# Optimization experiments

Hardware: AMD Instinct MI355X
Metric: run time of the kernel (lower is better)

The kernel has to match this reference:

```python
import jax, jax.numpy as jnp
import numpy as np

B, C, L = 4, 512, 4096

def setup_inputs() -> dict:
    key = jax.random.key(0)
    k1, k2, k3, k4 = jax.random.split(key, 4)
    proj_query = jax.random.normal(k1, (B, C, L), dtype=jnp.float32)
    proj_key = jax.random.normal(k2, (B, C, L), dtype=jnp.float32)
    proj_val = jax.random.normal(k3, (B, C, L), dtype=jnp.float32)
    # binary padding mask over key positions, broadcast over query axis
    padding_mask = (jax.random.uniform(k4, (B, 1, L)) < 0.9).astype(jnp.float32)
    return {"proj_query": proj_query, "proj_key": proj_key,
            "proj_val": proj_val, "padding_mask": padding_mask}

def reference(proj_query, proj_key, proj_val, padding_mask):
    c = proj_query.shape[1]
    # energy[b,i,j] = sum_c Q[b,c,i] * K[b,c,j]  -> (B, L1, L2)
    energy = jnp.einsum('bci,bcj->bij', proj_query, proj_key)
    attention = energy / jnp.sqrt(jnp.asarray(c, dtype=energy.dtype))
    attention = attention + jnp.log(padding_mask + 1e-6)
    attention = jax.nn.softmax(attention, axis=-1)
    attention = attention * padding_mask
    attention = attention.transpose(0, 2, 1)  # (B, L2, L1)
    out = jnp.einsum('bcj,bji->bci', proj_val, attention)  # (B, C, L1)
    return out, attention
```

## Files before the change

kernel.cpp:

```cpp
#include <hip/hip_runtime.h>

#define B_ 4
#define C_ 512
#define L_ 4096

typedef __attribute__((ext_vector_type(8))) short bf16x8;
typedef __attribute__((ext_vector_type(4))) float f32x4;

#define MFMA16(a, b, c) __builtin_amdgcn_mfma_f32_16x16x32_bf16(a, b, c, 0, 0, 0)

static __device__ __forceinline__ unsigned short f2bf_rne(float f) {
  unsigned u = __float_as_uint(f);
  u += 0x7FFFu + ((u >> 16) & 1u);
  return (unsigned short)(u >> 16);
}
static __device__ __forceinline__ unsigned pack_rne(float a, float b) {
  return (unsigned)f2bf_rne(a) | ((unsigned)f2bf_rne(b) << 16);
}
static __device__ __forceinline__ float bflo2f(unsigned w) {
  return __uint_as_float(w << 16);
}
static __device__ __forceinline__ float bfhi2f(unsigned w) {
  return __uint_as_float(w & 0xFFFF0000u);
}

static __device__ __forceinline__ void g2lds16(const unsigned short* g,
                                               unsigned short* l) {
  __builtin_amdgcn_global_load_lds(
      (const __attribute__((address_space(1))) unsigned int*)g,
      (__attribute__((address_space(3))) unsigned int*)l, 16, 0, 0);
}

__global__ __launch_bounds__(256) void transpose_cast_k(
    const float* __restrict__ Q, const float* __restrict__ K,
    unsigned short* __restrict__ Qt, unsigned short* __restrict__ Kt) {
  int zb = blockIdx.z;
  int b = zb >> 1;
  const float* src = ((zb & 1) ? K : Q) + (size_t)b * C_ * L_;
  unsigned short* dst = ((zb & 1) ? Kt : Qt) + (size_t)b * L_ * C_;
  int i0 = blockIdx.x * 64, c0 = blockIdx.y * 64;
  __shared__ float tile[64][65];
  int t = threadIdx.x;
  int cr = t >> 2, ig = (t & 3) * 16;
  const float* s = src + (size_t)(c0 + cr) * L_ + i0 + ig;
#pragma unroll
  for (int q = 0; q < 4; ++q) {
    float4 v = *(const float4*)(s + 4 * q);
    tile[cr][ig + 4 * q + 0] = v.x;
    tile[cr][ig + 4 * q + 1] = v.y;
    tile[cr][ig + 4 * q + 2] = v.z;
    tile[cr][ig + 4 * q + 3] = v.w;
  }
  __syncthreads();
  int ir = t >> 2, cg = (t & 3) * 16;
  unsigned wds[8];
#pragma unroll
  for (int k = 0; k < 8; ++k)
    wds[k] = pack_rne(tile[cg + 2 * k][ir], tile[cg + 2 * k + 1][ir]);
  unsigned short* d = dst + (size_t)(i0 + ir) * C_ + c0 + cg;
  uint4 o0, o1;
  o0.x = wds[0]; o0.y = wds[1]; o0.z = wds[2]; o0.w = wds[3];
  o1.x = wds[4]; o1.y = wds[5]; o1.z = wds[6]; o1.w = wds[7];
  *(uint4*)d = o0;
  *(uint4*)(d + 8) = o1;
}

__global__ __launch_bounds__(256) void cast_v_k(
    const float* __restrict__ V, const float* __restrict__ mask,
    unsigned short* __restrict__ Vb) {
  size_t idx = ((size_t)blockIdx.x * 256 + threadIdx.x) * 8;
  int b = (int)(idx >> 21);
  int j = (int)(idx & (L_ - 1));
  float4 v0 = *(const float4*)(V + idx);
  float4 v1 = *(const float4*)(V + idx + 4);
  const float* m = mask + (size_t)b * L_ + j;
  float4 m0 = *(const float4*)m;
  float4 m1 = *(const float4*)(m + 4);
  uint4 o;
  o.x = pack_rne(v0.x * m0.x, v0.y * m0.y);
  o.y = pack_rne(v0.z * m0.z, v0.w * m0.w);
  o.z = pack_rne(v1.x * m1.x, v1.y * m1.y);
  o.w = pack_rne(v1.z * m1.z, v1.w * m1.w);
  *(uint4*)(Vb + idx) = o;
}

__device__ __forceinline__ void gemm_8phase(
    const unsigned short* __restrict__ Ab,
    const unsigned short* __restrict__ Bb, int lda, int ldb, int Kdim,
    unsigned short* sA, unsigned short* sB, f32x4 (&acc)[8][4]) {
  const int t = threadIdx.x;
  const int lane = t & 63;
  const int quad = lane >> 4;
  const int l15 = lane & 15;
  const int w = t >> 6;
  const int wm = (w & 1) * 128;
  const int wn = (w >> 1) * 64;
  const int et = (t * 8) ^ (((t >> 5) & 1) << 4);
  const int srw = et >> 5;
  const int scl = et & 31;
  const int nt = Kdim >> 6;

  auto stage = [&](int nom, int hh) {
    int st = nom < nt ? nom : nt - 1;
    int db = nom & 1;
    int h = hh & 1;
    const unsigned short* g;
    unsigned short* l;
    if (hh < 2) {
      g = Bb + (size_t)(h * 128 + srw) * ldb + st * 64 + scl;
      l = sB + db * 16384 + h * 4096 + t * 8;
    } else {
      g = Ab + (size_t)(h * 128 + srw) * lda + st * 64 + scl;
      l = sA + db * 16384 + h * 4096 + t * 8;
    }
    g2lds16(g, l);
    g2lds16(g + 32, l + 8192);
  };
  auto rd = [&](const unsigned short* s, int db, int kc, int row) -> bf16x8 {
    int e = db * 16384 + kc * 8192 + row * 32 + quad * 8;
    e ^= ((e >> 8) & 1) << 4;
    return *(const bf16x8*)(s + e);
  };

  bf16x8 aF[4][2], b0[2][2], b1[2][2];
  auto rdA4 = [&](int db, int mbase) {
#pragma unroll
    for (int m = 0; m < 4; ++m)
#pragma unroll
      for (int kc = 0; kc < 2; ++kc)
        aF[m][kc] = rd(sA, db, kc, wm + (mbase + m) * 16 + l15);
  };
  auto rdB2 = [&](bf16x8 (&bf)[2][2], int db, int nbase) {
#pragma unroll
    for (int n = 0; n < 2; ++n)
#pragma unroll
      for (int kc = 0; kc < 2; ++kc)
        bf[n][kc] = rd(sB, db, kc, wn + (nbase + n) * 16 + l15);
  };
  auto mfma8 = [&](bf16x8 (&bf)[2][2], int mo, int no) {
    __builtin_amdgcn_s_setprio(1);
#pragma unroll
    for (int m = 0; m < 4; ++m)
#pragma unroll
      for (int n = 0; n < 2; ++n) {
        acc[mo + m][no + n] = MFMA16(aF[m][0], bf[n][0], acc[mo + m][no + n]);
        acc[mo + m][no + n] = MFMA16(aF[m][1], bf[n][1], acc[mo + m][no + n]);
      }
    __builtin_amdgcn_s_setprio(0);
  };

#define BAR_() __builtin_amdgcn_s_barrier()
#define LGKM0_() asm volatile("s_waitcnt lgkmcnt(0)" ::: "memory")
#define VM6_() asm volatile("s_waitcnt vmcnt(6)" ::: "memory")
#define SCHED0_() __builtin_amdgcn_sched_barrier(0)

  stage(0, 0); stage(0, 1); stage(0, 2); stage(0, 3);
  asm volatile("s_waitcnt vmcnt(4)" ::: "memory");
  stage(1, 0); stage(1, 1); stage(1, 2);
  asm volatile("s_waitcnt vmcnt(6)" ::: "memory");
  BAR_();

  const int ni = nt >> 1;
  for (int i = 0; i < ni; ++i) {
    const int X = 2 * i;
    rdA4(0, 0); rdB2(b0, 0, 0); rdB2(b1, 0, 2);
    stage(X + 1, 3);
    BAR_(); LGKM0_();
    mfma8(b0, 0, 0);
    BAR_();
    stage(X + 2, 0);
    BAR_();
    mfma8(b1, 0, 2);
    BAR_();
    rdA4(0, 4);
    stage(X + 2, 1);
    BAR_(); LGKM0_();
    mfma8(b0, 4, 0);
    BAR_();
    stage(X + 2, 2);
    VM6_(); BAR_();
    mfma8(b1, 4, 2);
    BAR_(); SCHED0_();
    rdA4(1, 0); rdB2(b0, 1, 0); rdB2(b1, 1, 2);
    stage(X + 2, 3);
    BAR_(); LGKM0_();
    mfma8(b0, 0, 0);
    BAR_();
    stage(X + 3, 0);
    BAR_();
    mfma8(b1, 0, 2);
    BAR_();
    rdA4(1, 4);
    stage(X + 3, 1);
    BAR_(); LGKM0_();
    mfma8(b0, 4, 0);
    BAR_();
    stage(X + 3, 2);
    VM6_(); BAR_();
    mfma8(b1, 4, 2);
    BAR_(); SCHED0_();
  }
  asm volatile("s_waitcnt vmcnt(0)" ::: "memory");
}

__global__ __launch_bounds__(512, 2) void gemm1_8p_k(
    const unsigned short* __restrict__ Qt, const unsigned short* __restrict__ Kt,
    const float* __restrict__ mask, unsigned short* __restrict__ t0,
    unsigned short* __restrict__ t1, unsigned short* __restrict__ t2,
    unsigned short* __restrict__ t3, float* __restrict__ rowsum) {
  __shared__ unsigned short sA[32768];
  __shared__ unsigned short sB[32768];
  int flat = blockIdx.x + (blockIdx.y << 4) + (blockIdx.z << 8);
  int swz = (flat & 7) * 128 + (flat >> 3);
  int bx = swz & 15, by = (swz >> 4) & 15, b = swz >> 8;
  unsigned short* tbb = (b == 0) ? t0 : (b == 1) ? t1 : (b == 2) ? t2 : t3;
  int i0 = by * 256, j0 = bx * 256;
  f32x4 acc[8][4] = {};
  gemm_8phase(Qt + (size_t)b * L_ * C_ + (size_t)i0 * C_,
              Kt + (size_t)b * L_ * C_ + (size_t)j0 * C_, C_, C_, C_, sA, sB,
              acc);
  int t = threadIdx.x;
  int lane = t & 63;
  int quad = lane >> 4;
  int l15 = lane & 15;
  int w = t >> 6;
  int wm = (w & 1) * 128;
  int wn = (w >> 1) * 64;
  const float scale = 0.04419417382415922f;
  float lm[4], mv[4];
#pragma unroll
  for (int n = 0; n < 4; ++n) {
    int j = j0 + wn + n * 16 + l15;
    float m = mask[(size_t)b * L_ + j];
    mv[n] = m;
    lm[n] = __logf(m + 1e-6f);
  }
  float rs[8][4];
#pragma unroll
  for (int m = 0; m < 8; ++m)
#pragma unroll
    for (int r = 0; r < 4; ++r) rs[m][r] = 0.f;
#pragma unroll
  for (int m = 0; m < 8; ++m) {
    int irow = i0 + wm + m * 16 + quad * 4;
#pragma unroll
    for (int r = 0; r < 4; ++r) {
      size_t ro = (size_t)(irow + r) * L_;
#pragma unroll
      for (int n = 0; n < 4; ++n) {
        float x = fminf(acc[m][n][r] * scale + lm[n], 60.f);
        float tv = __expf(x);
        rs[m][r] += tv;
        tbb[ro + j0 + wn + n * 16 + l15] = f2bf_rne(tv * mv[n]);
      }
    }
  }
#pragma unroll
  for (int mm = 1; mm < 16; mm <<= 1)
#pragma unroll
    for (int m = 0; m < 8; ++m)
#pragma unroll
      for (int r = 0; r < 4; ++r) rs[m][r] += __shfl_xor(rs[m][r], mm, 64);
  if (l15 == 0) {
    float* rb = rowsum + (size_t)b * L_ + i0 + wm;
#pragma unroll
    for (int m = 0; m < 8; ++m)
#pragma unroll
      for (int r = 0; r < 4; ++r)
        atomicAdd(&rb[m * 16 + quad * 4 + r], rs[m][r]);
  }
}

__global__ __launch_bounds__(512, 2) void gemm2_8p_k(
    const unsigned short* __restrict__ Vb, const unsigned short* __restrict__ t0,
    const unsigned short* __restrict__ t1, const unsigned short* __restrict__ t2,
    const unsigned short* __restrict__ t3, const float* __restrict__ rowsum,
    float* __restrict__ out, float* __restrict__ out2) {
  __shared__ unsigned short sA[32768];
  __shared__ unsigned short sB[32768];
  int flat = blockIdx.x + (blockIdx.y << 4) + (blockIdx.z << 5);
  int swz = (flat & 7) * 32 + (flat >> 3);
  int ix = swz & 15, cy = (swz >> 4) & 1, z = swz >> 5;
  int b = z & 3, ks = z >> 2;
  const unsigned short* tbb =
      (b == 0) ? t0 : (b == 1) ? t1 : (b == 2) ? t2 : t3;
  int i0 = ix * 256, c0 = cy * 256;
  f32x4 acc[8][4] = {};
  gemm_8phase(Vb + (size_t)b * C_ * L_ + (size_t)c0 * L_ + ks * (L_ / 2),
              tbb + (size_t)i0 * L_ + ks * (L_ / 2), L_, L_, L_ / 2, sA, sB,
              acc);
  int t = threadIdx.x;
  int lane = t & 63;
  int quad = lane >> 4;
  int l15 = lane & 15;
  int w = t >> 6;
  int wm = (w & 1) * 128;
  int wn = (w >> 1) * 64;
  float invv[4];
#pragma unroll
  for (int n = 0; n < 4; ++n)
    invv[n] = 1.0f / rowsum[(size_t)b * L_ + i0 + wn + n * 16 + l15];
  float* ob = (ks ? out2 : out) + (size_t)b * C_ * L_;
#pragma unroll
  for (int m = 0; m < 8; ++m) {
    int crow = c0 + wm + m * 16 + quad * 4;
#pragma unroll
    for (int r = 0; r < 4; ++r) {
      size_t ro = (size_t)(crow + r) * L_;
#pragma unroll
      for (int n = 0; n < 4; ++n)
        ob[ro + i0 + wn + n * 16 + l15] = acc[m][n][r] * invv[n];
    }
  }
}

__global__ __launch_bounds__(256) void combine_out_k(
    float* __restrict__ out, const float* __restrict__ out2) {
  size_t idx = ((size_t)blockIdx.x * 256 + threadIdx.x) * 8;
  float4 a0 = *(const float4*)(out + idx);
  float4 a1 = *(const float4*)(out + idx + 4);
  float4 b0 = *(const float4*)(out2 + idx);
  float4 b1 = *(const float4*)(out2 + idx + 4);
  a0.x += b0.x; a0.y += b0.y; a0.z += b0.z; a0.w += b0.w;
  a1.x += b1.x; a1.y += b1.y; a1.z += b1.z; a1.w += b1.w;
  *(float4*)(out + idx) = a0;
  *(float4*)(out + idx + 4) = a1;
}

__global__ __launch_bounds__(256) void finalize_all_k(
    const unsigned short* __restrict__ tb, const float* __restrict__ rowsum,
    float* __restrict__ attn) {
  int b = blockIdx.z;
  const unsigned short* src = tb + (size_t)b * L_ * L_;
  const float* rs = rowsum + (size_t)b * L_;
  float* dst = attn + (size_t)b * L_ * L_;
  int jt = blockIdx.x, it = blockIdx.y;
  __shared__ float tileT[64][65];
  int t = threadIdx.x;
  int r = t >> 2, cg = (t & 3) * 16;
  int i = it * 64 + r;
  float inv = 1.0f / rs[i];
  const unsigned short* sp = src + (size_t)i * L_ + jt * 64 + cg;
  uint4 u0 = *(const uint4*)sp;
  uint4 u1 = *(const uint4*)(sp + 8);
  const unsigned* w0 = (const unsigned*)&u0;
  const unsigned* w1 = (const unsigned*)&u1;
#pragma unroll
  for (int k = 0; k < 4; ++k) {
    tileT[cg + 2 * k + 0][r] = bflo2f(w0[k]) * inv;
    tileT[cg + 2 * k + 1][r] = bfhi2f(w0[k]) * inv;
    tileT[cg + 8 + 2 * k + 0][r] = bflo2f(w1[k]) * inv;
    tileT[cg + 8 + 2 * k + 1][r] = bfhi2f(w1[k]) * inv;
  }
  __syncthreads();
  float* dp = dst + (size_t)(jt * 64 + r) * L_ + it * 64 + cg;
#pragma unroll
  for (int q = 0; q < 4; ++q) {
    float4 o;
    o.x = tileT[r][cg + 4 * q + 0];
    o.y = tileT[r][cg + 4 * q + 1];
    o.z = tileT[r][cg + 4 * q + 2];
    o.w = tileT[r][cg + 4 * q + 3];
    *(float4*)(dp + 4 * q) = o;
  }
}

__device__ __forceinline__ void gemm_mainloop64(
    const unsigned short* Ab, const unsigned short* Bb, int lda, int ldb,
    int Kdim, unsigned short* sA, unsigned short* sB, f32x4 acc[4][4]) {
  int t = threadIdx.x;
  const unsigned short* pA[4];
  const unsigned short* pB[4];
#pragma unroll
  for (int c = 0; c < 4; ++c) {
    int e = t * 8 + c * 2048;
    int kc = e >> 12;
    int rem = e & 4095;
    int row = rem >> 5;
    int col = rem & 31;
    int off = kc * 32 + col;
    pA[c] = Ab + (size_t)row * lda + off;
    pB[c] = Bb + (size_t)row * ldb + off;
  }
  int lane = t & 63;
  int quad = lane >> 4;
  int l15 = lane & 15;
  int w = t >> 6;
  int wm = (w & 1) * 64;
  int wn = (w >> 1) * 64;
  for (int kk = 0; kk < Kdim; kk += 64) {
    __syncthreads();
#pragma unroll
    for (int c = 0; c < 4; ++c) g2lds16(pA[c] + kk, sA + t * 8 + c * 2048);
#pragma unroll
    for (int c = 0; c < 4; ++c) g2lds16(pB[c] + kk, sB + t * 8 + c * 2048);
    __syncthreads();
#pragma unroll
    for (int kc = 0; kc < 2; ++kc) {
      bf16x8 aF[4], bF[4];
#pragma unroll
      for (int ti = 0; ti < 4; ++ti)
        aF[ti] = *(const bf16x8*)(sA + kc * 4096 +
                                  (wm + ti * 16 + l15) * 32 + quad * 8);
#pragma unroll
      for (int tj = 0; tj < 4; ++tj)
        bF[tj] = *(const bf16x8*)(sB + kc * 4096 +
                                  (wn + tj * 16 + l15) * 32 + quad * 8);
#pragma unroll
      for (int ti = 0; ti < 4; ++ti)
#pragma unroll
        for (int tj = 0; tj < 4; ++tj)
          acc[ti][tj] = MFMA16(aF[ti], bF[tj], acc[ti][tj]);
    }
  }
}

__global__ __launch_bounds__(256) void gemm1_bf_k(
    const unsigned short* __restrict__ Qt, const unsigned short* __restrict__ Kt,
    const float* __restrict__ mask, unsigned short* __restrict__ t0,
    unsigned short* __restrict__ t1, unsigned short* __restrict__ t2,
    unsigned short* __restrict__ t3, float* __restrict__ rowsum) {
  int b = blockIdx.z;
  unsigned short* tbb = (b == 0) ? t0 : (b == 1) ? t1 : (b == 2) ? t2 : t3;
  int i0 = blockIdx.y * 128;
  int j0 = blockIdx.x * 128;
  __shared__ unsigned short sA[8192];
  __shared__ unsigned short sB[8192];
  f32x4 acc[4][4] = {};
  gemm_mainloop64(Qt + (size_t)b * L_ * C_ + (size_t)i0 * C_,
                  Kt + (size_t)b * L_ * C_ + (size_t)j0 * C_, C_, C_, C_, sA,
                  sB, acc);
  int t = threadIdx.x;
  int lane = t & 63;
  int quad = lane >> 4;
  int l15 = lane & 15;
  int w = t >> 6;
  int wm = (w & 1) * 64;
  int wn = (w >> 1) * 64;
  const float scale = 0.04419417382415922f;
  float lm[4], mv[4];
#pragma unroll
  for (int tj = 0; tj < 4; ++tj) {
    int j = j0 + wn + tj * 16 + l15;
    float m = mask[(size_t)b * L_ + j];
    mv[tj] = m;
    lm[tj] = __logf(m + 1e-6f);
  }
  float rs[16];
#pragma unroll
  for (int q = 0; q < 16; ++q) rs[q] = 0.f;
#pragma unroll
  for (int ti = 0; ti < 4; ++ti) {
    int irow = i0 + wm + ti * 16 + quad * 4;
#pragma unroll
    for (int r = 0; r < 4; ++r) {
      size_t ro = (size_t)(irow + r) * L_;
#pragma unroll
      for (int tj = 0; tj < 4; ++tj) {
        float x = fminf(acc[ti][tj][r] * scale + lm[tj], 60.f);
        float tv = __expf(x);
        rs[ti * 4 + r] += tv;
        tbb[ro + j0 + wn + tj * 16 + l15] = f2bf_rne(tv * mv[tj]);
      }
    }
  }
#pragma unroll
  for (int m = 1; m < 16; m <<= 1)
#pragma unroll
    for (int q = 0; q < 16; ++q) rs[q] += __shfl_xor(rs[q], m, 64);
  if (l15 == 0) {
    float* rb = rowsum + (size_t)b * L_ + i0 + wm;
#pragma unroll
    for (int ti = 0; ti < 4; ++ti)
#pragma unroll
      for (int r = 0; r < 4; ++r)
        atomicAdd(&rb[ti * 16 + quad * 4 + r], rs[ti * 4 + r]);
  }
}

__global__ __launch_bounds__(256) void gemm2_bf_k(
    const unsigned short* __restrict__ Vb, const unsigned short* __restrict__ t0,
    const unsigned short* __restrict__ t1, const unsigned short* __restrict__ t2,
    const unsigned short* __restrict__ t3, const float* __restrict__ rowsum,
    float* __restrict__ out) {
  int z = blockIdx.z;
  int b = z & 3;
  int ks = z >> 2;
  const unsigned short* tbb =
      (b == 0) ? t0 : (b == 1) ? t1 : (b == 2) ? t2 : t3;
  int c0 = blockIdx.y * 128;
  int i0 = blockIdx.x * 128;
  __shared__ unsigned short sA[8192];
  __shared__ unsigned short sB[8192];
  f32x4 acc[4][4] = {};
  gemm_mainloop64(Vb + (size_t)b * C_ * L_ + (size_t)c0 * L_ + ks * (L_ / 2),
                  tbb + (size_t)i0 * L_ + ks * (L_ / 2), L_, L_, L_ / 2, sA, sB,
                  acc);
  int t = threadIdx.x;
  int lane = t & 63;
  int quad = lane >> 4;
  int l15 = lane & 15;
  int w = t >> 6;
  int wm = (w & 1) * 64;
  int wn = (w >> 1) * 64;
  float invv[4];
#pragma unroll
  for (int tj = 0; tj < 4; ++tj)
    invv[tj] = 1.0f / rowsum[(size_t)b * L_ + i0 + wn + tj * 16 + l15];
  float* ob = out + (size_t)b * C_ * L_;
#pragma unroll
  for (int ti = 0; ti < 4; ++ti) {
    int crow = c0 + wm + ti * 16 + quad * 4;
#pragma unroll
    for (int r = 0; r < 4; ++r) {
      size_t ro = (size_t)(crow + r) * L_;
#pragma unroll
      for (int tj = 0; tj < 4; ++tj)
        atomicAdd(&ob[ro + i0 + wn + tj * 16 + l15],
                  acc[ti][tj][r] * invv[tj]);
    }
  }
}

extern "C" void kernel_launch(void* const* d_in, const int* in_sizes, int n_in,
                              void* d_out, int out_size, void* d_ws,
                              size_t ws_size, hipStream_t stream) {
  const float* Q = (const float*)d_in[0];
  const float* K = (const float*)d_in[1];
  const float* V = (const float*)d_in[2];
  const float* mask = (const float*)d_in[3];

  float* out = (float*)d_out;
  float* attn = out + (size_t)B_ * C_ * L_;

  const size_t NQ = (size_t)B_ * L_ * C_;
  const size_t SLOT = (size_t)L_ * L_;
  unsigned short* Qt = (unsigned short*)d_ws;
  unsigned short* Kt = Qt + NQ;
  unsigned short* Vb = Kt + NQ;
  float* rowsum = (float*)(Vb + NQ);
  unsigned short* wtail = (unsigned short*)(rowsum + (size_t)B_ * L_);

  const size_t need1 =
      NQ * 2 * 3 + (size_t)B_ * L_ * 4 + (size_t)B_ * SLOT * 2 + NQ * 4;

  hipMemsetAsync(rowsum, 0, (size_t)B_ * L_ * sizeof(float), stream);
  transpose_cast_k<<<dim3(L_ / 64, C_ / 64, B_ * 2), 256, 0, stream>>>(Q, K, Qt,
                                                                       Kt);
  cast_v_k<<<dim3((B_ * C_ * L_) / 2048), 256, 0, stream>>>(V, mask, Vb);

  if (ws_size >= need1) {
    unsigned short* tb = wtail;
    float* out2 = (float*)(tb + (size_t)B_ * SLOT);
    gemm1_8p_k<<<dim3(16, 16, B_), 512, 0, stream>>>(
        Qt, Kt, mask, tb, tb + SLOT, tb + 2 * SLOT, tb + 3 * SLOT, rowsum);
    gemm2_8p_k<<<dim3(16, 2, B_ * 2), 512, 0, stream>>>(
        Vb, tb, tb + SLOT, tb + 2 * SLOT, tb + 3 * SLOT, rowsum, out, out2);
    combine_out_k<<<dim3((B_ * C_ * L_) / 2048), 256, 0, stream>>>(out, out2);
    finalize_all_k<<<dim3(64, 64, B_), 256, 0, stream>>>(tb, rowsum, attn);
  } else {
    unsigned short* tb0 = (unsigned short*)(attn + 2 * SLOT);
    unsigned short* tb1 = (unsigned short*)(attn + 3 * SLOT);
    unsigned short* tb2 = (unsigned short*)(attn + 3 * SLOT + SLOT / 2);
    unsigned short* tb3 = wtail;
    hipMemsetAsync(out, 0, (size_t)B_ * C_ * L_ * sizeof(float), stream);
    gemm1_bf_k<<<dim3(L_ / 128, L_ / 128, B_), 256, 0, stream>>>(
        Qt, Kt, mask, tb0, tb1, tb2, tb3, rowsum);
    gemm2_bf_k<<<dim3(L_ / 128, C_ / 128, B_ * 2), 256, 0, stream>>>(
        Vb, tb0, tb1, tb2, tb3, rowsum, out);
    finalize_all_k<<<dim3(64, 64, 1), 256, 0, stream>>>(tb0, rowsum, attn);
    finalize_all_k<<<dim3(64, 64, 1), 256, 0, stream>>>(tb1, rowsum + L_,
                                                        attn + SLOT);
    finalize_all_k<<<dim3(64, 64, 1), 256, 0, stream>>>(tb2, rowsum + 2 * L_,
                                                        attn + 2 * SLOT);
    finalize_all_k<<<dim3(64, 64, 1), 256, 0, stream>>>(tb3, rowsum + 3 * L_,
                                                        attn + 3 * SLOT);
  }
}
```

Baseline: 662.7 us.

## Replace split-K gemm2 with data-parallel 128x256 tiles, drop combine kernel

The second GEMM (V times attention) no longer splits K into two halves written to separate buffers and summed by a combine kernel. It now uses smaller 128x256 output tiles over the full K range, 256 workgroups mapped by XCD so each batch stays on paired XCDs, and its own double-buffered pipeline with finer-grained vmcnt waits. This removes the extra out2 write, the combine pass and its workspace, at the cost of less reuse per tile and a new hand-tuned staging schedule.

```diff
diff --git a/kernel.cpp b/kernel.cpp
--- a/kernel.cpp
+++ b/kernel.cpp
@@ -30,6 +30,10 @@
       (const __attribute__((address_space(1))) unsigned int*)g,
       (__attribute__((address_space(3))) unsigned int*)l, 16, 0, 0);
 }
+
+#define BAR_() __builtin_amdgcn_s_barrier()
+#define LGKM0_() asm volatile("s_waitcnt lgkmcnt(0)" ::: "memory")
+#define VMW_(N) asm volatile("s_waitcnt vmcnt(" #N ")" ::: "memory")
 
 __global__ __launch_bounds__(256) void transpose_cast_k(
     const float* __restrict__ Q, const float* __restrict__ K,
@@ -149,11 +153,6 @@
     __builtin_amdgcn_s_setprio(0);
   };
 
-#define BAR_() __builtin_amdgcn_s_barrier()
-#define LGKM0_() asm volatile("s_waitcnt lgkmcnt(0)" ::: "memory")
-#define VM6_() asm volatile("s_waitcnt vmcnt(6)" ::: "memory")
-#define SCHED0_() __builtin_amdgcn_sched_barrier(0)
-
   stage(0, 0); stage(0, 1); stage(0, 2); stage(0, 3);
   asm volatile("s_waitcnt vmcnt(4)" ::: "memory");
   stage(1, 0); stage(1, 1); stage(1, 2);
@@ -178,9 +177,9 @@
     mfma8(b0, 4, 0);
     BAR_();
     stage(X + 2, 2);
-    VM6_(); BAR_();
+    VMW_(6); BAR_();
     mfma8(b1, 4, 2);
-    BAR_(); SCHED0_();
+    BAR_(); __builtin_amdgcn_sched_barrier(0);
     rdA4(1, 0); rdB2(b0, 1, 0); rdB2(b1, 1, 2);
     stage(X + 2, 3);
     BAR_(); LGKM0_();
@@ -196,9 +195,9 @@
     mfma8(b0, 4, 0);
     BAR_();
     stage(X + 3, 2);
-    VM6_(); BAR_();
+    VMW_(6); BAR_();
     mfma8(b1, 4, 2);
-    BAR_(); SCHED0_();
+    BAR_(); __builtin_amdgcn_sched_barrier(0);
   }
   asm volatile("s_waitcnt vmcnt(0)" ::: "memory");
 }
@@ -271,60 +270,153 @@
   }
 }
 
-__global__ __launch_bounds__(512, 2) void gemm2_8p_k(
+__global__ __launch_bounds__(512, 2) void gemm2_dp_k(
     const unsigned short* __restrict__ Vb, const unsigned short* __restrict__ t0,
     const unsigned short* __restrict__ t1, const unsigned short* __restrict__ t2,
     const unsigned short* __restrict__ t3, const float* __restrict__ rowsum,
-    float* __restrict__ out, float* __restrict__ out2) {
-  __shared__ unsigned short sA[32768];
+    float* __restrict__ out) {
+  __shared__ unsigned short sA[16384];
   __shared__ unsigned short sB[32768];
-  int flat = blockIdx.x + (blockIdx.y << 4) + (blockIdx.z << 5);
-  int swz = (flat & 7) * 32 + (flat >> 3);
-  int ix = swz & 15, cy = (swz >> 4) & 1, z = swz >> 5;
-  int b = z & 3, ks = z >> 2;
+  int wgid = blockIdx.x;
+  int xcd = wgid & 7;
+  int b = xcd >> 1;
+  int ixh = xcd & 1;
+  int s = wgid >> 3;
+  int ixl = s >> 2;
+  int cy = s & 3;
+  int ix = ixh * 8 + ixl;
+  int i0 = ix * 256;
+  int c0 = cy * 128;
   const unsigned short* tbb =
       (b == 0) ? t0 : (b == 1) ? t1 : (b == 2) ? t2 : t3;
-  int i0 = ix * 256, c0 = cy * 256;
-  f32x4 acc[8][4] = {};
-  gemm_8phase(Vb + (size_t)b * C_ * L_ + (size_t)c0 * L_ + ks * (L_ / 2),
-              tbb + (size_t)i0 * L_ + ks * (L_ / 2), L_, L_, L_ / 2, sA, sB,
-              acc);
-  int t = threadIdx.x;
-  int lane = t & 63;
-  int quad = lane >> 4;
-  int l15 = lane & 15;
-  int w = t >> 6;
-  int wm = (w & 1) * 128;
-  int wn = (w >> 1) * 64;
+  const unsigned short* Ab = Vb + (size_t)b * C_ * L_ + (size_t)c0 * L_;
+  const unsigned short* Bb = tbb + (size_t)i0 * L_;
+
+  const int t = threadIdx.x;
+  const int lane = t & 63;
+  const int quad = lane >> 4;
+  const int l15 = lane & 15;
+  const int w = t >> 6;
+  const int wm = (w & 1) * 64;
+  const int wn16 = (w >> 1) * 16;
+  const int et = (t * 8) ^ (((t >> 5) & 1) << 4);
+  const int srw = et >> 5;
+  const int scl = et & 31;
+  const int nt = L_ >> 6;
+
+  auto stageA = [&](int nom) {
+    int st = nom < nt ? nom : nt - 1;
+    int db = nom & 1;
+#pragma unroll
+    for (int kc = 0; kc < 2; ++kc)
+      g2lds16(Ab + (size_t)srw * L_ + st * 64 + kc * 32 + scl,
+              sA + db * 8192 + kc * 4096 + t * 8);
+  };
+  auto stageB = [&](int nom, int kc, int rh) {
+    int st = nom < nt ? nom : nt - 1;
+    int db = nom & 1;
+    g2lds16(Bb + (size_t)(rh * 128 + srw) * L_ + st * 64 + kc * 32 + scl,
+            sB + db * 16384 + kc * 8192 + rh * 4096 + t * 8);
+  };
+
+  bf16x8 aF[4][2], bF[2];
+  auto rdA = [&](int db) {
+#pragma unroll
+    for (int m = 0; m < 4; ++m)
+#pragma unroll
+      for (int kc = 0; kc < 2; ++kc) {
+        int e = db * 8192 + kc * 4096 + (wm + m * 16 + l15) * 32 + quad * 8;
+        e ^= ((e >> 8) & 1) << 4;
+        aF[m][kc] = *(const bf16x8*)(sA + e);
+      }
+  };
+  auto rdB = [&](int db, int n) {
+#pragma unroll
+    for (int kc = 0; kc < 2; ++kc) {
+      int e = db * 16384 + kc * 8192 + (n * 64 + wn16 + l15) * 32 + quad * 8;
+      e ^= ((e >> 8) & 1) << 4;
+      bF[kc] = *(const bf16x8*)(sB + e);
+    }
+  };
+
+  f32x4 acc[4][4] = {};
+  auto mfma8 = [&](int n) {
+    __builtin_amdgcn_s_setprio(1);
+#pragma unroll
+    for (int m = 0; m < 4; ++m) {
+      acc[m][n] = MFMA16(aF[m][0], bF[0], acc[m][n]);
+      acc[m][n] = MFMA16(aF[m][1], bF[1], acc[m][n]);
+    }
+    __builtin_amdgcn_s_setprio(0);
+  };
+
+  stageA(0);
+  stageB(0, 0, 0); stageB(0, 1, 0); stageB(0, 0, 1);
+  stageA(1);
+  stageB(0, 1, 1); stageB(1, 0, 0); stageB(1, 1, 0);
+
+  const int ni = nt >> 1;
+  for (int i = 0; i < ni; ++i) {
+    const int X = 2 * i;
+    stageB(X + 1, 0, 1);
+    VMW_(7); BAR_();
+    rdA(0); rdB(0, 0); LGKM0_();
+    mfma8(0);
+    BAR_();
+    stageA(X + 2); stageB(X + 1, 1, 1);
+    VMW_(10); BAR_();
+    rdB(0, 1); LGKM0_();
+    mfma8(1);
+    BAR_();
+    stageB(X + 2, 0, 0);
+    VMW_(7); BAR_();
+    rdB(0, 2); LGKM0_();
+    mfma8(2);
+    BAR_();
+    stageB(X + 2, 1, 0);
+    VMW_(8); BAR_();
+    rdB(0, 3); LGKM0_();
+    mfma8(3);
+    BAR_();
+    stageB(X + 2, 0, 1);
+    VMW_(7); BAR_();
+    rdA(1); rdB(1, 0); LGKM0_();
+    mfma8(0);
+    BAR_();
+    stageA(X + 3); stageB(X + 2, 1, 1);
+    VMW_(10); BAR_();
+    rdB(1, 1); LGKM0_();
+    mfma8(1);
+    BAR_();
+    stageB(X + 3, 0, 0);
+    VMW_(7); BAR_();
+    rdB(1, 2); LGKM0_();
+    mfma8(2);
+    BAR_();
+    stageB(X + 3, 1, 0);
+    VMW_(8); BAR_();
+    rdB(1, 3); LGKM0_();
+    mfma8(3);
+    BAR_();
+  }
+  asm volatile("s_waitcnt vmcnt(0)" ::: "memory");
+
   float invv[4];
 #pragma unroll
   for (int n = 0; n < 4; ++n)
-    invv[n] = 1.0f / rowsum[(size_t)b * L_ + i0 + wn + n * 16 + l15];
-  float* ob = (ks ? out2 : out) + (size_t)b * C_ * L_;
-#pragma unroll
-  for (int m = 0; m < 8; ++m) {
+    invv[n] = 1.0f / rowsum[(size_t)b * L_ + i0 + n * 64 + wn16 + l15];
+  float* ob = out + (size_t)b * C_ * L_;
+#pragma unroll
+  for (int m = 0; m < 4; ++m) {
     int crow = c0 + wm + m * 16 + quad * 4;
 #pragma unroll
     for (int r = 0; r < 4; ++r) {
       size_t ro = (size_t)(crow + r) * L_;
 #pragma unroll
       for (int n = 0; n < 4; ++n)
-        ob[ro + i0 + wn + n * 16 + l15] = acc[m][n][r] * invv[n];
-    }
-  }
-}
-
-__global__ __launch_bounds__(256) void combine_out_k(
-    float* __restrict__ out, const float* __restrict__ out2) {
-  size_t idx = ((size_t)blockIdx.x * 256 + threadIdx.x) * 8;
-  float4 a0 = *(const float4*)(out + idx);
-  float4 a1 = *(const float4*)(out + idx + 4);
-  float4 b0 = *(const float4*)(out2 + idx);
-  float4 b1 = *(const float4*)(out2 + idx + 4);
-  a0.x += b0.x; a0.y += b0.y; a0.z += b0.z; a0.w += b0.w;
-  a1.x += b1.x; a1.y += b1.y; a1.z += b1.z; a1.w += b1.w;
-  *(float4*)(out + idx) = a0;
-  *(float4*)(out + idx + 4) = a1;
+        ob[ro + i0 + n * 64 + wn16 + l15] = acc[m][n][r] * invv[n];
+    }
+  }
 }
 
 __global__ __launch_bounds__(256) void finalize_all_k(
@@ -541,8 +633,7 @@
   float* rowsum = (float*)(Vb + NQ);
   unsigned short* wtail = (unsigned short*)(rowsum + (size_t)B_ * L_);
 
-  const size_t need1 =
-      NQ * 2 * 3 + (size_t)B_ * L_ * 4 + (size_t)B_ * SLOT * 2 + NQ * 4;
+  const size_t need1 = NQ * 2 * 3 + (size_t)B_ * L_ * 4 + (size_t)B_ * SLOT * 2;
 
   hipMemsetAsync(rowsum, 0, (size_t)B_ * L_ * sizeof(float), stream);
   transpose_cast_k<<<dim3(L_ / 64, C_ / 64, B_ * 2), 256, 0, stream>>>(Q, K, Qt,
@@ -551,12 +642,10 @@
 
   if (ws_size >= need1) {
     unsigned short* tb = wtail;
-    float* out2 = (float*)(tb + (size_t)B_ * SLOT);
     gemm1_8p_k<<<dim3(16, 16, B_), 512, 0, stream>>>(
         Qt, Kt, mask, tb, tb + SLOT, tb + 2 * SLOT, tb + 3 * SLOT, rowsum);
-    gemm2_8p_k<<<dim3(16, 2, B_ * 2), 512, 0, stream>>>(
-        Vb, tb, tb + SLOT, tb + 2 * SLOT, tb + 3 * SLOT, rowsum, out, out2);
-    combine_out_k<<<dim3((B_ * C_ * L_) / 2048), 256, 0, stream>>>(out, out2);
+    gemm2_dp_k<<<dim3(256), 512, 0, stream>>>(
+        Vb, tb, tb + SLOT, tb + 2 * SLOT, tb + 3 * SLOT, rowsum, out);
     finalize_all_k<<<dim3(64, 64, B_), 256, 0, stream>>>(tb, rowsum, attn);
   } else {
     unsigned short* tb0 = (unsigned short*)(attn + 2 * SLOT);
```

Result: slower. 684.3 us (+3.3%).
